# Performance work log

Measured on AMD Instinct MI355X. Metric: run time of the kernel, lower is better.

## Reference

```python
import jax, jax.numpy as jnp
import numpy as np

N_SYS, N_ANC = 2, 2
NQ = N_SYS + N_ANC          # 4 qubits total
DIM = 2 ** NQ               # 16-dim statevector
NUM_LAYERS = 2

# --- constant gate structure (PennyLane convention: wire 0 is the MSB) ---

def _cnot_full(control, target):
    U = np.zeros((DIM, DIM), dtype=np.float32)
    for i in range(DIM):
        cbit = (i >> (NQ - 1 - control)) & 1
        j = i ^ ((1 << (NQ - 1 - target)) * cbit)
        U[j, i] = 1.0
    return U

# BasicEntanglerLayers ring: CNOT(0,1), CNOT(1,2), CNOT(2,3), CNOT(3,0) in sequence
_ring = np.eye(DIM, dtype=np.float32)
for _c in range(NQ):
    _ring = _cnot_full(_c, (_c + 1) % NQ) @ _ring
CNOT_RING = jnp.asarray(_ring)

# PauliZ eigenvalues on measurement_qubit = 1 (second-most-significant wire)
_Z1 = jnp.asarray(np.array([(-1.0) ** ((i >> (NQ - 2)) & 1) for i in range(DIM)],
                            dtype=np.float32))

# --- parameterized part ---

def _ry(theta):
    # RY is real: [[cos t/2, -sin t/2], [sin t/2, cos t/2]]
    c, s = jnp.cos(theta * 0.5), jnp.sin(theta * 0.5)
    return jnp.stack([jnp.stack([c, -s]), jnp.stack([s, c])])

def _layer_unitary(w):
    # one BasicEntangler layer: RY(w[q]) on each wire, then the CNOT ring
    U = _ry(w[0])
    for q in range(1, NQ):
        U = jnp.kron(U, _ry(w[q]))
    return CNOT_RING @ U

def _circuit_unitary(U_params, Udagger_params):
    # entangling layers (0,1) then 'disentangling' with layer order flipped (1,0)
    weights = jnp.concatenate([U_params, Udagger_params[::-1]], axis=0)  # (4, NQ)
    C = jnp.eye(DIM, dtype=U_params.dtype)
    for l in range(2 * NUM_LAYERS):
        C = _layer_unitary(weights[l]) @ C
    return C


def setup_inputs() -> dict:
    key = jax.random.key(0)
    k1, k2, k3, k4, k5, k6 = jax.random.split(key, 6)
    B = 1048576
    return {
        "x": jax.random.normal(k1, (B, 1), dtype=jnp.float32),
        "h_prev": jax.random.uniform(k2, (B, 4), dtype=jnp.float32),
        "W_in": jax.random.normal(k3, (4, 1), dtype=jnp.float32),
        "b_in": jax.random.normal(k4, (4,), dtype=jnp.float32),
        "U_params": jax.random.uniform(k5, (2, 4), dtype=jnp.float32),
        "Udagger_params": jax.random.uniform(k6, (2, 4), dtype=jnp.float32),
    }


def reference(x, h_prev, W_in, b_in, U_params, Udagger_params):
    B = x.shape[0]
    # input projection + normalization (replicates proj / ||proj + 1e-12||)
    proj = x @ W_in.T + b_in                                   # (B, 4)
    inp = proj / jnp.linalg.norm(proj + 1e-12, axis=-1, keepdims=True)
    # AmplitudeEmbedding(kron(input_state, h_prev), normalize=True)
    joint = (inp[:, :, None] * h_prev[:, None, :]).reshape(B, DIM)   # (B, 16)
    joint = joint / jnp.linalg.norm(joint, axis=-1, keepdims=True)
    # all gates (RY, CNOT) are real -> state stays real; fuse circuit into one 16x16
    C = _circuit_unitary(U_params, Udagger_params)
    psi = joint @ C.T                                          # (B, 16)
    p = psi * psi                                              # |amplitude|^2
    # diag of reduced density matrix on ancilla wires [2,3]: trace out system wires
    h_next = p.reshape(B, 2 ** N_SYS, 2 ** N_ANC).sum(axis=1)  # (B, 4)
    # expval PauliZ(wire 1)
    output = p @ _Z1                                           # (B,)
    return h_next, output
```

## Files before the change

### kernel.cpp

```cpp
#include <hip/hip_runtime.h>


__device__ __forceinline__ int ring_perm(int k) {
  int b0 = (k >> 3) & 1, b1 = (k >> 2) & 1, b2 = (k >> 1) & 1, b3 = k & 1;
  b1 ^= b0; b2 ^= b1; b3 ^= b2; b0 ^= b3;
  return (b0 << 3) | (b1 << 2) | (b2 << 1) | b3;
}

__global__ __launch_bounds__(256) void build_consts_kernel(
    const float* __restrict__ W_in, const float* __restrict__ b_in,
    const float* __restrict__ U, const float* __restrict__ Ud,
    float* __restrict__ ws) {
  __shared__ float M[16][16];
  __shared__ float Lm[16][16];
  const int t = threadIdx.x;
  const int i = t >> 4, j = t & 15;
  const int pi = ring_perm(i);

  float ang[4][4];
#pragma unroll
  for (int q = 0; q < 4; ++q) {
    ang[0][q] = U[q];
    ang[1][q] = U[4 + q];
    ang[2][q] = Ud[4 + q];
    ang[3][q] = Ud[q];
  }

  {
    float kel = 1.f;
#pragma unroll
    for (int q = 0; q < 4; ++q) {
      float c = cosf(0.5f * ang[0][q]);
      float s = sinf(0.5f * ang[0][q]);
      int iq = (i >> (3 - q)) & 1, jq = (j >> (3 - q)) & 1;
      kel *= (iq == jq) ? c : (iq ? s : -s);
    }
    M[pi][j] = kel;
  }
  __syncthreads();

  for (int l = 1; l < 4; ++l) {
    float kel = 1.f;
#pragma unroll
    for (int q = 0; q < 4; ++q) {
      float c = cosf(0.5f * ang[l][q]);
      float s = sinf(0.5f * ang[l][q]);
      int iq = (i >> (3 - q)) & 1, jq = (j >> (3 - q)) & 1;
      kel *= (iq == jq) ? c : (iq ? s : -s);
    }
    Lm[pi][j] = kel;
    __syncthreads();
    float acc = 0.f;
#pragma unroll
    for (int k = 0; k < 16; ++k) acc += Lm[i][k] * M[k][j];
    __syncthreads();
    M[i][j] = acc;
    __syncthreads();
  }

  if (t < 64) {
    const int r = t >> 2, k = t & 3;
    float a = 0.f, bb = 0.f;
#pragma unroll
    for (int q = 0; q < 4; ++q) {
      float c = M[r][4 * q + k];
      a = fmaf(W_in[q], c, a);
      bb = fmaf(b_in[q], c, bb);
    }
    ws[r * 4 + k] = a;
    ws[64 + r * 4 + k] = bb;
  }
  if (t == 0) {
    float qa = 0.f, qb = 0.f, qc = 0.f;
#pragma unroll
    for (int q = 0; q < 4; ++q) {
      qa = fmaf(W_in[q], W_in[q], qa);
      qb = fmaf(2.f * W_in[q], b_in[q], qb);
      qc = fmaf(b_in[q], b_in[q], qc);
    }
    ws[128] = qa; ws[129] = qb; ws[130] = qc;
  }
}

__global__ __launch_bounds__(256) void qlstm_kernel(
    const float* __restrict__ x, const float4* __restrict__ h_prev,
    const float* __restrict__ AB, float4* __restrict__ h_next,
    float* __restrict__ outp, int B) {
  int gid = blockIdx.x * 256 + threadIdx.x;
  if (gid >= B) return;
  float xv = x[gid];
  float4 h = h_prev[gid];
  float nh2 = fmaf(h.x, h.x, fmaf(h.y, h.y, fmaf(h.z, h.z, h.w * h.w)));
  float qa = AB[128], qb = AB[129], qc = AB[130];
  float nu2 = fmaf(fmaf(qa, xv, qb), xv, qc);
  float inv2 = __builtin_amdgcn_rcpf(nu2 * nh2);

  float hn[4] = {0.f, 0.f, 0.f, 0.f};
  float po = 0.f;
#pragma unroll
  for (int r = 0; r < 16; ++r) {
    float ar = fmaf(AB[r * 4 + 0], h.x,
               fmaf(AB[r * 4 + 1], h.y,
               fmaf(AB[r * 4 + 2], h.z, AB[r * 4 + 3] * h.w)));
    float br = fmaf(AB[64 + r * 4 + 0], h.x,
               fmaf(AB[64 + r * 4 + 1], h.y,
               fmaf(AB[64 + r * 4 + 2], h.z, AB[64 + r * 4 + 3] * h.w)));
    float tr = fmaf(xv, ar, br);
    float s = tr * tr;
    hn[r & 3] += s;
    po += ((r >> 2) & 1) ? -s : s;
  }
  float4 o;
  o.x = hn[0] * inv2;
  o.y = hn[1] * inv2;
  o.z = hn[2] * inv2;
  o.w = hn[3] * inv2;
  h_next[gid] = o;
  outp[gid] = po * inv2;
}

extern "C" void kernel_launch(void* const* d_in, const int* in_sizes, int n_in,
                              void* d_out, int out_size, void* d_ws, size_t ws_size,
                              hipStream_t stream) {
  const float* x  = (const float*)d_in[0];
  const float* h  = (const float*)d_in[1];
  const float* W  = (const float*)d_in[2];
  const float* bi = (const float*)d_in[3];
  const float* U  = (const float*)d_in[4];
  const float* Ud = (const float*)d_in[5];
  float* ws = (float*)d_ws;
  const int B = in_sizes[0];
  float* h_next = (float*)d_out;
  float* out1   = (float*)d_out + 4 * (size_t)B;

  build_consts_kernel<<<1, 256, 0, stream>>>(W, bi, U, Ud, ws);
  qlstm_kernel<<<(B + 255) / 256, 256, 0, stream>>>(
      x, (const float4*)h, ws, (float4*)h_next, out1, B);
}
```

Measured before the change: 87.13 us.

## Fuse constant-building into main kernel with per-block recompute, four rows per thread

Removes the separate single-block kernel that builds the fused circuit constants. Each block of the main kernel now recomputes the 16x16 circuit unitary and projection coefficients in shared memory, then processes four rows per thread. This drops a launch and its serialization gap and keeps the coefficients in LDS instead of global memory. In exchange every block (1024 of them) repeats the trig and matrix-product prologue with several barriers, which adds latency before any memory traffic starts.

```diff
diff --git a/kernel.cpp b/kernel.cpp
--- a/kernel.cpp
+++ b/kernel.cpp
@@ -1,5 +1,7 @@
 #include <hip/hip_runtime.h>
 
+
+#define ROWS_PER_BLOCK 1024
 
 __device__ __forceinline__ int ring_perm(int k) {
   int b0 = (k >> 3) & 1, b1 = (k >> 2) & 1, b2 = (k >> 1) & 1, b3 = k & 1;
@@ -7,116 +9,143 @@
   return (b0 << 3) | (b1 << 2) | (b2 << 1) | b3;
 }
 
-__global__ __launch_bounds__(256) void build_consts_kernel(
+__global__ __launch_bounds__(256) void qlstm_fused(
+    const float* __restrict__ x, const float4* __restrict__ h_prev,
     const float* __restrict__ W_in, const float* __restrict__ b_in,
     const float* __restrict__ U, const float* __restrict__ Ud,
-    float* __restrict__ ws) {
+    float4* __restrict__ h_next, float* __restrict__ outp, int B) {
   __shared__ float M[16][16];
   __shared__ float Lm[16][16];
+  __shared__ float4 sA[16];
+  __shared__ float4 sB[16];
+  __shared__ float sQ[3];
+
   const int t = threadIdx.x;
-  const int i = t >> 4, j = t & 15;
-  const int pi = ring_perm(i);
-
-  float ang[4][4];
-#pragma unroll
-  for (int q = 0; q < 4; ++q) {
-    ang[0][q] = U[q];
-    ang[1][q] = U[4 + q];
-    ang[2][q] = Ud[4 + q];
-    ang[3][q] = Ud[q];
-  }
 
   {
-    float kel = 1.f;
+    const int i = t >> 4, j = t & 15;
+    const int pi = ring_perm(i);
+
+    float ang[4][4];
 #pragma unroll
     for (int q = 0; q < 4; ++q) {
-      float c = cosf(0.5f * ang[0][q]);
-      float s = sinf(0.5f * ang[0][q]);
-      int iq = (i >> (3 - q)) & 1, jq = (j >> (3 - q)) & 1;
-      kel *= (iq == jq) ? c : (iq ? s : -s);
+      ang[0][q] = U[q];
+      ang[1][q] = U[4 + q];
+      ang[2][q] = Ud[4 + q];
+      ang[3][q] = Ud[q];
     }
-    M[pi][j] = kel;
-  }
-  __syncthreads();
 
-  for (int l = 1; l < 4; ++l) {
-    float kel = 1.f;
+    {
+      float kel = 1.f;
 #pragma unroll
-    for (int q = 0; q < 4; ++q) {
-      float c = cosf(0.5f * ang[l][q]);
-      float s = sinf(0.5f * ang[l][q]);
-      int iq = (i >> (3 - q)) & 1, jq = (j >> (3 - q)) & 1;
-      kel *= (iq == jq) ? c : (iq ? s : -s);
+      for (int q = 0; q < 4; ++q) {
+        float c = cosf(0.5f * ang[0][q]);
+        float s = sinf(0.5f * ang[0][q]);
+        int iq = (i >> (3 - q)) & 1, jq = (j >> (3 - q)) & 1;
+        kel *= (iq == jq) ? c : (iq ? s : -s);
+      }
+      M[pi][j] = kel;
     }
-    Lm[pi][j] = kel;
     __syncthreads();
-    float acc = 0.f;
+
+    for (int l = 1; l < 4; ++l) {
+      float kel = 1.f;
 #pragma unroll
-    for (int k = 0; k < 16; ++k) acc += Lm[i][k] * M[k][j];
-    __syncthreads();
-    M[i][j] = acc;
+      for (int q = 0; q < 4; ++q) {
+        float c = cosf(0.5f * ang[l][q]);
+        float s = sinf(0.5f * ang[l][q]);
+        int iq = (i >> (3 - q)) & 1, jq = (j >> (3 - q)) & 1;
+        kel *= (iq == jq) ? c : (iq ? s : -s);
+      }
+      Lm[pi][j] = kel;
+      __syncthreads();
+      float acc = 0.f;
+#pragma unroll
+      for (int k = 0; k < 16; ++k) acc += Lm[i][k] * M[k][j];
+      __syncthreads();
+      M[i][j] = acc;
+      __syncthreads();
+    }
+
+    if (t < 64) {
+      const int r = t >> 2, k = t & 3;
+      float a = 0.f, bb = 0.f;
+#pragma unroll
+      for (int q = 0; q < 4; ++q) {
+        float c = M[r][4 * q + k];
+        a = fmaf(W_in[q], c, a);
+        bb = fmaf(b_in[q], c, bb);
+      }
+      ((float*)sA)[t] = a;
+      ((float*)sB)[t] = bb;
+    }
+    if (t == 0) {
+      float qa = 0.f, qb = 0.f, qc = 0.f;
+#pragma unroll
+      for (int q = 0; q < 4; ++q) {
+        qa = fmaf(W_in[q], W_in[q], qa);
+        qb = fmaf(2.f * W_in[q], b_in[q], qb);
+        qc = fmaf(b_in[q], b_in[q], qc);
+      }
+      sQ[0] = qa; sQ[1] = qb; sQ[2] = qc;
+    }
     __syncthreads();
   }
 
-  if (t < 64) {
-    const int r = t >> 2, k = t & 3;
-    float a = 0.f, bb = 0.f;
+  const int base = blockIdx.x * ROWS_PER_BLOCK + t;
+  const float qa = sQ[0], qb = sQ[1], qc = sQ[2];
+
+  float xv[4];
+  float4 h[4];
+  bool ok[4];
 #pragma unroll
-    for (int q = 0; q < 4; ++q) {
-      float c = M[r][4 * q + k];
-      a = fmaf(W_in[q], c, a);
-      bb = fmaf(b_in[q], c, bb);
-    }
-    ws[r * 4 + k] = a;
-    ws[64 + r * 4 + k] = bb;
+  for (int j = 0; j < 4; ++j) {
+    const int row = base + j * 256;
+    ok[j] = row < B;
+    xv[j] = ok[j] ? x[row] : 0.f;
+    h[j] = ok[j] ? h_prev[row] : make_float4(0.f, 0.f, 0.f, 0.f);
   }
-  if (t == 0) {
-    float qa = 0.f, qb = 0.f, qc = 0.f;
+
+  float inv2[4];
 #pragma unroll
-    for (int q = 0; q < 4; ++q) {
-      qa = fmaf(W_in[q], W_in[q], qa);
-      qb = fmaf(2.f * W_in[q], b_in[q], qb);
-      qc = fmaf(b_in[q], b_in[q], qc);
-    }
-    ws[128] = qa; ws[129] = qb; ws[130] = qc;
+  for (int j = 0; j < 4; ++j) {
+    float nh2 = fmaf(h[j].x, h[j].x,
+                fmaf(h[j].y, h[j].y,
+                fmaf(h[j].z, h[j].z, h[j].w * h[j].w)));
+    float nu2 = fmaf(fmaf(qa, xv[j], qb), xv[j], qc);
+    inv2[j] = __builtin_amdgcn_rcpf(nu2 * nh2);
   }
-}
 
-__global__ __launch_bounds__(256) void qlstm_kernel(
-    const float* __restrict__ x, const float4* __restrict__ h_prev,
-    const float* __restrict__ AB, float4* __restrict__ h_next,
-    float* __restrict__ outp, int B) {
-  int gid = blockIdx.x * 256 + threadIdx.x;
-  if (gid >= B) return;
-  float xv = x[gid];
-  float4 h = h_prev[gid];
-  float nh2 = fmaf(h.x, h.x, fmaf(h.y, h.y, fmaf(h.z, h.z, h.w * h.w)));
-  float qa = AB[128], qb = AB[129], qc = AB[130];
-  float nu2 = fmaf(fmaf(qa, xv, qb), xv, qc);
-  float inv2 = __builtin_amdgcn_rcpf(nu2 * nh2);
-
-  float hn[4] = {0.f, 0.f, 0.f, 0.f};
-  float po = 0.f;
+  float hn[4][4] = {};
+  float po[4] = {0.f, 0.f, 0.f, 0.f};
 #pragma unroll
   for (int r = 0; r < 16; ++r) {
-    float ar = fmaf(AB[r * 4 + 0], h.x,
-               fmaf(AB[r * 4 + 1], h.y,
-               fmaf(AB[r * 4 + 2], h.z, AB[r * 4 + 3] * h.w)));
-    float br = fmaf(AB[64 + r * 4 + 0], h.x,
-               fmaf(AB[64 + r * 4 + 1], h.y,
-               fmaf(AB[64 + r * 4 + 2], h.z, AB[64 + r * 4 + 3] * h.w)));
-    float tr = fmaf(xv, ar, br);
-    float s = tr * tr;
-    hn[r & 3] += s;
-    po += ((r >> 2) & 1) ? -s : s;
+    const float4 a = sA[r];
+    const float4 bm = sB[r];
+#pragma unroll
+    for (int j = 0; j < 4; ++j) {
+      float ar = fmaf(a.x, h[j].x,
+                 fmaf(a.y, h[j].y,
+                 fmaf(a.z, h[j].z, a.w * h[j].w)));
+      float br = fmaf(bm.x, h[j].x,
+                 fmaf(bm.y, h[j].y,
+                 fmaf(bm.z, h[j].z, bm.w * h[j].w)));
+      float tr = fmaf(xv[j], ar, br);
+      float s = tr * tr;
+      hn[j][r & 3] += s;
+      po[j] += ((r >> 2) & 1) ? -s : s;
+    }
   }
-  float4 o;
-  o.x = hn[0] * inv2;
-  o.y = hn[1] * inv2;
-  o.z = hn[2] * inv2;
-  o.w = hn[3] * inv2;
-  h_next[gid] = o;
-  outp[gid] = po * inv2;
+
+#pragma unroll
+  for (int j = 0; j < 4; ++j) {
+    if (ok[j]) {
+      const int row = base + j * 256;
+      h_next[row] = make_float4(hn[j][0] * inv2[j], hn[j][1] * inv2[j],
+                                hn[j][2] * inv2[j], hn[j][3] * inv2[j]);
+      outp[row] = po[j] * inv2[j];
+    }
+  }
 }
 
 extern "C" void kernel_launch(void* const* d_in, const int* in_sizes, int n_in,
@@ -128,12 +157,11 @@
   const float* bi = (const float*)d_in[3];
   const float* U  = (const float*)d_in[4];
   const float* Ud = (const float*)d_in[5];
-  float* ws = (float*)d_ws;
   const int B = in_sizes[0];
   float* h_next = (float*)d_out;
   float* out1   = (float*)d_out + 4 * (size_t)B;
 
-  build_consts_kernel<<<1, 256, 0, stream>>>(W, bi, U, Ud, ws);
-  qlstm_kernel<<<(B + 255) / 256, 256, 0, stream>>>(
-      x, (const float4*)h, ws, (float4*)h_next, out1, B);
+  const int grid = (B + ROWS_PER_BLOCK - 1) / ROWS_PER_BLOCK;
+  qlstm_fused<<<grid, 256, 0, stream>>>(
+      x, (const float4*)h, W, bi, U, Ud, (float4*)h_next, out1, B);
 }
```

Result: slower. 92.98 us (+6.7%).
